# Optimization experiments

Measured on AMD Instinct MI355X. Metric: run time of the kernel, lower is better.

## Reference

```python
import jax, jax.numpy as jnp
import numpy as np

B = 32768   # batch
F = 32      # per-node feature dim
H = 256     # hidden width
M = 4       # modules per node
OUT = 8     # final output dim
INIT_W = 0.003
B_INIT = 0.1


def _lin(k, din, dout):
    # fanin_init-style uniform weights, bias filled with 0.1 (hidden layers)
    s = 1.0 / np.sqrt(din)
    W = jax.random.uniform(k, (M, din, dout), jnp.float32, -s, s)
    b = jnp.full((M, dout), B_INIT, jnp.float32)
    return W, b


def setup_inputs() -> dict:
    key = jax.random.key(0)
    ks = jax.random.split(key, 16)
    feats = jax.random.normal(ks[0], (B, 4 * F), jnp.float32)
    idx = jax.random.randint(ks[1], (B, 4), 0, M)
    onehots = jax.nn.one_hot(idx, M, dtype=jnp.float32).reshape(B, 4 * M)
    input_val = jnp.concatenate([feats, onehots], axis=1)  # [B,144]

    W00, b00 = _lin(ks[2], F, H)        # node0 post layer 0
    W01, b01 = _lin(ks[3], H, H)        # node0 post layer 1
    Wpre1, bpre1 = _lin(ks[4], F, H)    # node1 pre
    Wpost1, bpost1 = _lin(ks[5], 2 * H, H)  # node1 interface (prev 256 + own 256)
    Wpre2, bpre2 = _lin(ks[6], F, H)
    Wpost2, bpost2 = _lin(ks[7], 2 * H, H)
    Wpre3, bpre3 = _lin(ks[8], F, H)
    Wpost3, bpost3 = _lin(ks[9], 2 * H, H)
    # final output layer: uniform(-init_w, init_w) for W and b, identity act
    Wfin3 = jax.random.uniform(ks[10], (M, H, OUT), jnp.float32, -INIT_W, INIT_W)
    bfin3 = jax.random.uniform(ks[11], (M, OUT), jnp.float32, -INIT_W, INIT_W)
    return dict(input_val=input_val,
                W00=W00, b00=b00, W01=W01, b01=b01,
                Wpre1=Wpre1, bpre1=bpre1, Wpost1=Wpost1, bpost1=bpost1,
                Wpre2=Wpre2, bpre2=bpre2, Wpost2=Wpost2, bpost2=bpost2,
                Wpre3=Wpre3, bpre3=bpre3, Wpost3=Wpost3, bpost3=bpost3,
                Wfin3=Wfin3, bfin3=bfin3)


def _select(h, onehot):
    # per-row pick of the assigned module's output: [B,M,D],[B,M] -> [B,D]
    return jnp.einsum('bmo,bm->bo', h, onehot)


def reference(input_val, W00, b00, W01, b01,
              Wpre1, bpre1, Wpost1, bpost1,
              Wpre2, bpre2, Wpost2, bpost2,
              Wpre3, bpre3, Wpost3, bpost3,
              Wfin3, bfin3):
    feat = lambda j: input_val[:, j * F:(j + 1) * F]
    oh = lambda j: input_val[:, 4 * F + j * M: 4 * F + (j + 1) * M]

    # node 0: two hidden layers, module-dispatched (dense-all-modules + one-hot combine)
    h = jax.nn.relu(jnp.einsum('bi,mio->bmo', feat(0), W00) + b00)
    h = jax.nn.relu(jnp.einsum('bmi,mio->bmo', h, W01) + b01)
    x = _select(h, oh(0))  # [B,H]

    def node(x_prev, fj, ohj, Wpre, bpre, Wpost, bpost):
        hp = jax.nn.relu(jnp.einsum('bi,mio->bmo', fj, Wpre) + bpre)
        # interface layer consumes concat([x_prev, hp]); split the weight to
        # avoid materializing [B,M,2H]
        hq = jax.nn.relu(jnp.einsum('bi,mio->bmo', x_prev, Wpost[:, :H, :])
                         + jnp.einsum('bmi,mio->bmo', hp, Wpost[:, H:, :])
                         + bpost)
        return hq  # [B,M,H]

    x = _select(node(x, feat(1), oh(1), Wpre1, bpre1, Wpost1, bpost1), oh(1))
    x = _select(node(x, feat(2), oh(2), Wpre2, bpre2, Wpost2, bpost2), oh(2))

    h3 = node(x, feat(3), oh(3), Wpre3, bpre3, Wpost3, bpost3)  # [B,M,H]
    out = jnp.einsum('bmi,mio->bmo', h3, Wfin3) + bfin3          # final linear, identity act
    return _select(out, oh(3))  # [B,OUT]
```

## Files before the change

kernel.cpp:

```cpp
#include <hip/hip_runtime.h>

#define NB 32768
#define MAXTILE 768
#define ROWS 64
#define NT 4
#define XHS 536

typedef short s8v __attribute__((ext_vector_type(8)));
typedef short s4v __attribute__((ext_vector_type(4)));
typedef float f4v __attribute__((ext_vector_type(4)));
typedef unsigned short u16;
typedef unsigned short u16x4 __attribute__((ext_vector_type(4)));
typedef unsigned int u32;
typedef unsigned char u8;

__device__ __forceinline__ float bf2f(u16 u) { return __uint_as_float(((u32)u) << 16); }
__device__ __forceinline__ u16 f2bf(float f) {
    u32 x = __float_as_uint(f);
    x += 0x7FFFu + ((x >> 16) & 1u);
    return (u16)(x >> 16);
}
__device__ __forceinline__ s8v ld8(const u16* p) { return *reinterpret_cast<const s8v*>(p); }

#define MFMA16(a, b, c) __builtin_amdgcn_mfma_f32_16x16x32_bf16((a), (b), (c), 0, 0, 0)

template <int N> struct IC { static constexpr int v = N; };

__device__ __forceinline__ void detect_flag(const void* input, int tid, int* shflag)
{
    if (tid < 64) {
        u32 w = ((const u32*)input)[tid];
        u32 h0 = w & 0xFFFFu;
        u32 e0 = (h0 >> 7) & 0xFFu;
        bool plaus = (h0 == 0u) || (e0 >= 96u && e0 <= 143u);
        unsigned long long m = __ballot(plaus);
        if (tid == 0) *shflag = (__popcll(m) >= 48) ? 1 : 0;
    }
}

struct RepArgs {
    const void* W01; const void* Wp[3]; const void* pre[4]; const void* fin;
    const void* bias[9];
    u16 *rPre, *rW01, *rWp[3], *rFin, *cbias;
};

__global__ __launch_bounds__(256) void prepA_kernel(const void* __restrict__ inputv,
                                                    int* __restrict__ gcnt,
                                                    int* __restrict__ perm2,
                                                    RepArgs R)
{
    __shared__ int lcnt[256];
    __shared__ int sBase[256];
    __shared__ u16 T[8192];
    __shared__ int shmisc;
    int tid = threadIdx.x;
    int b = blockIdx.x;
    detect_flag(inputv, tid, &shmisc);
    __syncthreads();
    int flag = shmisc;

    if (b < 128) {
        lcnt[tid] = 0;
        __syncthreads();
        int row = (b << 8) + tid;
        const u32* in32 = (const u32*)inputv;
        const u16* in16 = (const u16*)inputv;
        int key = 0;
        if (flag) {
#pragma unroll
            for (int j = 0; j < 4; j++) {
                u16x4 v = *(const u16x4*)(in16 + row * 144 + 128 + j * 4);
                int m = v[1] ? 1 : (v[2] ? 2 : (v[3] ? 3 : 0));
                key |= m << (j << 1);
            }
        } else {
#pragma unroll
            for (int j = 0; j < 4; j++) {
                const u32* p = in32 + row * 144 + 128 + j * 4;
                u32 v1 = p[1], v2 = p[2], v3 = p[3];
                int m = v1 ? 1 : (v2 ? 2 : (v3 ? 3 : 0));
                key |= m << (j << 1);
            }
        }
        int loc = atomicAdd(&lcnt[key], 1);
        __syncthreads();
        int c = lcnt[tid];
        sBase[tid] = c ? atomicAdd(&gcnt[tid], c) : 0;
        __syncthreads();
        int slot = sBase[key] + loc;
        if (slot < 512) perm2[(key << 9) + slot] = row;
        return;
    }

    int rb = b - 128;
    const void* src = nullptr; u16* dst = nullptr; int K = 0, k0 = 0, mrow = 0;
    if (rb < 32) {
        int m = rb >> 3, s = rb & 7;
        src = R.W01; dst = R.rW01 + (m * 8 + s) * 8192; K = 256; k0 = s * 32; mrow = m;
    } else if (rb < 224) {
        int idx = rb - 32, mat = idx >> 6, r = idx & 63, m = r >> 4, s = r & 15;
        src = R.Wp[mat]; dst = R.rWp[mat] + (m * 16 + s) * 8192; K = 512; k0 = s * 32; mrow = m;
    } else if (rb < 240) {
        int idx = rb - 224, mat = idx >> 2, m = idx & 3;
        src = R.pre[mat]; dst = R.rPre + (mat * 4 + m) * 8192; K = 32; k0 = 0; mrow = m;
    } else if (rb < 244) {
        int m = rb - 240;
        const u16* s16 = (const u16*)R.fin;
        const float* s32 = (const float*)R.fin;
        for (int i = tid; i < 2048; i += 256) {
            int si = (m * 256 + (i >> 3)) * 8 + (i & 7);
            T[i] = flag ? s16[si] : f2bf(s32[si]);
        }
        __syncthreads();
        u16* d = R.rFin + m * 4096;
        for (int i = tid; i < 4096; i += 256) {
            int s = i >> 9, lane = (i >> 3) & 63, j = i & 7;
            int q = lane >> 4, l16 = lane & 15;
            int k = s * 32 + q * 8 + j;
            d[i] = (l16 < 8) ? T[k * 8 + l16] : (u16)0;
        }
        return;
    } else {
        const int sz[9] = {1024,1024,1024,1024,1024,1024,1024,1024,32};
        const int of[9] = {0,1024,2048,3072,4096,5120,6144,7168,8192};
        for (int i = tid; i < 8224; i += 256) {
            int t = i, e = 0;
            while (t >= sz[e]) { t -= sz[e]; e++; }
            R.cbias[of[e] + t] = flag ? ((const u16*)R.bias[e])[t]
                                      : f2bf(((const float*)R.bias[e])[t]);
        }
        return;
    }
    const u16* s16 = (const u16*)src;
    const float* s32 = (const float*)src;
    for (int i = tid; i < 8192; i += 256) {
        int k = i >> 8, n = i & 255;
        int srcIdx = (mrow * K + k0 + k) * 256 + n;
        T[i] = flag ? s16[srcIdx] : f2bf(s32[srcIdx]);
    }
    __syncthreads();
    for (int i = tid; i < 8192; i += 256) {
        int mt = i >> 9, lane = (i >> 3) & 63, j = i & 7;
        int k = ((lane >> 4) << 3) + j, n = (mt << 4) + (lane & 15);
        dst[i] = T[(k << 8) + n];
    }
}

struct MainP { const u16 *rPre, *rW01, *rWp1, *rWp2, *rWp3, *rFin, *cbias; };

__global__ __launch_bounds__(512, 4) void main_kernel(
    const void* __restrict__ inRaw,
    const int* __restrict__ gcnt, const int* __restrict__ perm2,
    MainP P, void* __restrict__ outp)
{
    __shared__ __align__(16) u16 xh[ROWS * XHS];
    __shared__ int rowids[ROWS];
    __shared__ int shflag;
    __shared__ int sMeta[4];

    int tid = threadIdx.x;
    int lane = tid & 63, w = tid >> 6, quad = lane >> 4, l16 = lane & 15;

    int b = blockIdx.x;
    int t = ((b & 7) * (MAXTILE / 8)) + (b >> 3);

    detect_flag(inRaw, tid, &shflag);

    if (tid < 64) {
        int4 g = *(const int4*)(gcnt + tid * 4);
        int tot4[4] = {g.x, g.y, g.z, g.w};
        int tiles4[4], lsum = 0;
#pragma unroll
        for (int j = 0; j < 4; j++) { tiles4[j] = (tot4[j] + 63) >> 6; lsum += tiles4[j]; }
        int pre = lsum;
#pragma unroll
        for (int off = 1; off < 64; off <<= 1) {
            int v = __shfl_up(pre, off, 64);
            if (tid >= off) pre += v;
        }
        int run = pre - lsum;
#pragma unroll
        for (int j = 0; j < 4; j++) {
            if (t >= run && t < run + tiles4[j]) {
                sMeta[0] = tid * 4 + j;
                sMeta[1] = t - run;
                sMeta[2] = tot4[j];
            }
            run += tiles4[j];
        }
        if (tid == 63) sMeta[3] = pre;
    }
    __syncthreads();
    if (t >= sMeta[3]) return;
    int key = sMeta[0], tau = sMeta[1], tot = sMeta[2];
    int cntIn = tot - tau * ROWS; if (cntIn > ROWS) cntIn = ROWS;
    if (tid < ROWS) {
        int g = tid < cntIn ? tid : cntIn - 1;
        rowids[tid] = perm2[(key << 9) + tau * ROWS + g];
    }
    __syncthreads();

    int flag = shflag;
    int rows_[NT];
#pragma unroll
    for (int nt = 0; nt < NT; nt++) rows_[nt] = rowids[nt * 16 + l16];

    const u16* in16 = (const u16*)inRaw;
    const float* in32 = (const float*)inRaw;
    int mt0 = w << 1, mt1 = mt0 + 1;

    f4v acc0[NT], acc1[NT];

    auto gemm_run = [&](auto nc, const u16* Ab, int ks0) {
        constexpr int N = decltype(nc)::v;
        constexpr int D = (N > 8) ? 6 : 4;
        const u16* base0 = Ab + mt0 * 512 + lane * 8;
        const u16* base1 = Ab + mt1 * 512 + lane * 8;
        s8v A0[D], A1[D];
#pragma unroll
        for (int d = 0; d < D && d < N; d++) {
            A0[d] = ld8(base0 + d * 8192);
            A1[d] = ld8(base1 + d * 8192);
        }
        __syncthreads();
        __builtin_amdgcn_s_setprio(1);
#pragma unroll
        for (int s = 0; s < N; s++) {
            s8v c0 = A0[s % D], c1 = A1[s % D];
            if (s + D < N) {
                A0[s % D] = ld8(base0 + (s + D) * 8192);
                A1[s % D] = ld8(base1 + (s + D) * 8192);
            }
#pragma unroll
            for (int nt = 0; nt < NT; nt++) {
                s8v B = ld8(&xh[(nt * 16 + l16) * XHS + (ks0 + s) * 32 + quad * 8]);
                acc0[nt] = MFMA16(c0, B, acc0[nt]);
                acc1[nt] = MFMA16(c1, B, acc1[nt]);
            }
        }
        __builtin_amdgcn_s_setprio(0);
    };

    for (int node = 0; node < 4; node++) {
        int m = (key >> (node << 1)) & 3;

        s8v fb[NT];
#pragma unroll
        for (int nt = 0; nt < NT; nt++) {
            int off = rows_[nt] * 144 + (node << 5) + (quad << 3);
            if (flag) fb[nt] = ld8(in16 + off);
            else {
                f4v f0 = *(const f4v*)(in32 + off);
                f4v f1 = *(const f4v*)(in32 + off + 4);
                s8v r;
#pragma unroll
                for (int j = 0; j < 4; j++) { r[j] = (short)f2bf(f0[j]); r[4 + j] = (short)f2bf(f1[j]); }
                fb[nt] = r;
            }
        }

        const u16* preB = P.rPre + ((node << 2) + m) * 8192;
#pragma unroll
        for (int ci = 0; ci < 2; ci++) {
            int mt = mt0 + ci;
            s8v a = ld8(preB + mt * 512 + lane * 8);
            u16x4 bv = *(const u16x4*)(P.cbias + node * 2048 + m * 256 + mt * 16 + quad * 4);
            f4v bias;
#pragma unroll
            for (int r = 0; r < 4; r++) bias[r] = bf2f(bv[r]);
#pragma unroll
            for (int nt = 0; nt < NT; nt++) {
                f4v c = MFMA16(a, fb[nt], bias);
                s4v p;
#pragma unroll
                for (int r = 0; r < 4; r++) { float v = c[r] > 0.f ? c[r] : 0.f; p[r] = (short)f2bf(v); }
                *(s4v*)&xh[(nt * 16 + l16) * XHS + 256 + mt * 16 + quad * 4] = p;
            }
        }

        {
            u16x4 b0 = *(const u16x4*)(P.cbias + node * 2048 + 1024 + m * 256 + mt0 * 16 + quad * 4);
            u16x4 b1 = *(const u16x4*)(P.cbias + node * 2048 + 1024 + m * 256 + mt1 * 16 + quad * 4);
            f4v f0, f1;
#pragma unroll
            for (int r = 0; r < 4; r++) { f0[r] = bf2f(b0[r]); f1[r] = bf2f(b1[r]); }
#pragma unroll
            for (int nt = 0; nt < NT; nt++) { acc0[nt] = f0; acc1[nt] = f1; }
        }

        if (node == 0) gemm_run(IC<8>{},  P.rW01 + m * 8 * 8192, 8);
        else {
            const u16* WB = (node == 1 ? P.rWp1 : (node == 2 ? P.rWp2 : P.rWp3)) + m * 16 * 8192;
            gemm_run(IC<16>{}, WB, 0);
        }
        __syncthreads();

#pragma unroll
        for (int ci = 0; ci < 2; ci++) {
            int mt = mt0 + ci;
#pragma unroll
            for (int nt = 0; nt < NT; nt++) {
                f4v a = ci ? acc1[nt] : acc0[nt];
                s4v p;
#pragma unroll
                for (int r = 0; r < 4; r++) { float v = a[r] > 0.f ? a[r] : 0.f; p[r] = (short)f2bf(v); }
                *(s4v*)&xh[(nt * 16 + l16) * XHS + mt * 16 + quad * 4] = p;
            }
        }
    }
    __syncthreads();

    if (w < NT) {
        int m3 = (key >> 6) & 3;
        f4v c;
#pragma unroll
        for (int r = 0; r < 4; r++)
            c[r] = (quad < 2) ? bf2f(P.cbias[8192 + m3 * 8 + quad * 4 + r]) : 0.f;
#pragma unroll
        for (int s = 0; s < 8; s++) {
            s8v A = ld8(P.rFin + m3 * 4096 + s * 512 + lane * 8);
            s8v B = ld8(&xh[(w * 16 + l16) * XHS + s * 32 + quad * 8]);
            c = MFMA16(A, B, c);
        }
        int bidx = w * 16 + l16;
        if (quad < 2 && bidx < cntIn) {
            int row = rowids[bidx];
            if (flag) {
                s4v p;
#pragma unroll
                for (int r = 0; r < 4; r++) p[r] = (short)f2bf(c[r]);
                *(s4v*)((u16*)outp + row * 8 + quad * 4) = p;
            } else {
                *(f4v*)((float*)outp + row * 8 + quad * 4) = c;
            }
        }
    }
}

extern "C" void kernel_launch(void* const* d_in, const int* in_sizes, int n_in,
                              void* d_out, int out_size, void* d_ws, size_t ws_size,
                              hipStream_t stream)
{
    (void)in_sizes; (void)n_in; (void)out_size;
    const void* input  = d_in[0];
    const void* W00    = d_in[1];
    const void* b00    = d_in[2];
    const void* W01    = d_in[3];
    const void* b01    = d_in[4];
    const void* Wpre1  = d_in[5];
    const void* bpre1  = d_in[6];
    const void* Wpost1 = d_in[7];
    const void* bpost1 = d_in[8];
    const void* Wpre2  = d_in[9];
    const void* bpre2  = d_in[10];
    const void* Wpost2 = d_in[11];
    const void* bpost2 = d_in[12];
    const void* Wpre3  = d_in[13];
    const void* bpre3  = d_in[14];
    const void* Wpost3 = d_in[15];
    const void* bpost3 = d_in[16];
    const void* Wfin   = d_in[17];
    const void* bfin   = d_in[18];

    char* base = (char*)d_ws;
    size_t off = 0;
    auto alloc = [&](size_t bytes) -> char* {
        char* p = base + off;
        off += (bytes + 255) & ~(size_t)255;
        return p;
    };
    int*  gcnt      = (int*)alloc(256 * 4);
    int*  perm2     = (int*)alloc(256 * 512 * 4);
    u16*  cbias    = (u16*)alloc(8224 * 2);
    u16*  rPre     = (u16*)alloc(131072 * 2);
    u16*  rW01     = (u16*)alloc(262144 * 2);
    u16*  rWp1     = (u16*)alloc(524288 * 2);
    u16*  rWp2     = (u16*)alloc(524288 * 2);
    u16*  rWp3     = (u16*)alloc(524288 * 2);
    u16*  rFin     = (u16*)alloc(16384 * 2);
    if (off > ws_size) return;

    RepArgs R;
    R.W01 = W01; R.Wp[0] = Wpost1; R.Wp[1] = Wpost2; R.Wp[2] = Wpost3;
    R.pre[0] = W00; R.pre[1] = Wpre1; R.pre[2] = Wpre2; R.pre[3] = Wpre3;
    R.fin = Wfin;
    R.bias[0] = b00;   R.bias[1] = b01;
    R.bias[2] = bpre1; R.bias[3] = bpost1;
    R.bias[4] = bpre2; R.bias[5] = bpost2;
    R.bias[6] = bpre3; R.bias[7] = bpost3;
    R.bias[8] = bfin;
    R.rPre = rPre; R.rW01 = rW01;
    R.rWp[0] = rWp1; R.rWp[1] = rWp2; R.rWp[2] = rWp3;
    R.rFin = rFin; R.cbias = cbias;

    hipMemsetAsync(gcnt, 0, 256 * 4, stream);
    prepA_kernel<<<373, 256, 0, stream>>>(input, gcnt, perm2, R);

    MainP P;
    P.rPre = rPre; P.rW01 = rW01; P.rWp1 = rWp1; P.rWp2 = rWp2; P.rWp3 = rWp3;
    P.rFin = rFin; P.cbias = cbias;
    main_kernel<<<MAXTILE, 512, 0, stream>>>(input, gcnt, perm2, P, d_out);
}
```

Baseline: 191.3 us.

## Pre-pack bf16 features and store activations in MFMA-fragment LDS layout

```diff
diff --git a/kernel.cpp b/kernel.cpp
--- a/kernel.cpp
+++ b/kernel.cpp
@@ -4,7 +4,6 @@
 #define MAXTILE 768
 #define ROWS 64
 #define NT 4
-#define XHS 536
 
 typedef short s8v __attribute__((ext_vector_type(8)));
 typedef short s4v __attribute__((ext_vector_type(4)));
@@ -47,6 +46,7 @@
 __global__ __launch_bounds__(256) void prepA_kernel(const void* __restrict__ inputv,
                                                     int* __restrict__ gcnt,
                                                     int* __restrict__ perm2,
+                                                    u16* __restrict__ feats16,
                                                     RepArgs R)
 {
     __shared__ int lcnt[256];
@@ -89,6 +89,23 @@
         __syncthreads();
         int slot = sBase[key] + loc;
         if (slot < 512) perm2[(key << 9) + slot] = row;
+
+        int r0 = b << 8;
+        if (flag) {
+            for (int i = tid; i < 256 * 16; i += 256) {
+                int r = r0 + (i >> 4), j = (i & 15) << 3;
+                *(s8v*)(feats16 + ((size_t)r << 7) + j) = ld8(in16 + (size_t)r * 144 + j);
+            }
+        } else {
+            for (int i = tid; i < 256 * 32; i += 256) {
+                int r = r0 + (i >> 5), j = (i & 31) << 2;
+                f4v f = *(const f4v*)(in32 + (size_t)r * 144 + j);
+                s4v p;
+#pragma unroll
+                for (int q = 0; q < 4; q++) p[q] = (short)f2bf(f[q]);
+                *(s4v*)(feats16 + ((size_t)r << 7) + j) = p;
+            }
+        }
         return;
     }
 
@@ -146,14 +163,14 @@
     }
 }
 
-struct MainP { const u16 *rPre, *rW01, *rWp1, *rWp2, *rWp3, *rFin, *cbias; };
+struct MainP { const u16 *rPre, *rW01, *rWp1, *rWp2, *rWp3, *rFin, *cbias, *feats; };
 
 __global__ __launch_bounds__(512, 4) void main_kernel(
     const void* __restrict__ inRaw,
     const int* __restrict__ gcnt, const int* __restrict__ perm2,
     MainP P, void* __restrict__ outp)
 {
-    __shared__ __align__(16) u16 xh[ROWS * XHS];
+    __shared__ __align__(16) u16 xhB[32768];
     __shared__ int rowids[ROWS];
     __shared__ int shflag;
     __shared__ int sMeta[4];
@@ -205,15 +222,15 @@
 #pragma unroll
     for (int nt = 0; nt < NT; nt++) rows_[nt] = rowids[nt * 16 + l16];
 
-    const u16* in16 = (const u16*)inRaw;
-    const float* in32 = (const float*)inRaw;
+    const u16* feats = P.feats;
     int mt0 = w << 1, mt1 = mt0 + 1;
+    int stA = ((quad >> 1) * 16 + l16) * 8 + (quad & 1) * 4;
 
     f4v acc0[NT], acc1[NT];
 
     auto gemm_run = [&](auto nc, const u16* Ab, int ks0) {
         constexpr int N = decltype(nc)::v;
-        constexpr int D = (N > 8) ? 6 : 4;
+        constexpr int D = 4;
         const u16* base0 = Ab + mt0 * 512 + lane * 8;
         const u16* base1 = Ab + mt1 * 512 + lane * 8;
         s8v A0[D], A1[D];
@@ -233,7 +250,7 @@
             }
 #pragma unroll
             for (int nt = 0; nt < NT; nt++) {
-                s8v B = ld8(&xh[(nt * 16 + l16) * XHS + (ks0 + s) * 32 + quad * 8]);
+                s8v B = ld8(&xhB[((nt * 16 + ks0 + s) << 9) + lane * 8]);
                 acc0[nt] = MFMA16(c0, B, acc0[nt]);
                 acc1[nt] = MFMA16(c1, B, acc1[nt]);
             }
@@ -246,18 +263,8 @@
 
         s8v fb[NT];
 #pragma unroll
-        for (int nt = 0; nt < NT; nt++) {
-            int off = rows_[nt] * 144 + (node << 5) + (quad << 3);
-            if (flag) fb[nt] = ld8(in16 + off);
-            else {
-                f4v f0 = *(const f4v*)(in32 + off);
-                f4v f1 = *(const f4v*)(in32 + off + 4);
-                s8v r;
-#pragma unroll
-                for (int j = 0; j < 4; j++) { r[j] = (short)f2bf(f0[j]); r[4 + j] = (short)f2bf(f1[j]); }
-                fb[nt] = r;
-            }
-        }
+        for (int nt = 0; nt < NT; nt++)
+            fb[nt] = ld8(feats + ((size_t)rows_[nt] << 7) + (node << 5) + (quad << 3));
 
         const u16* preB = P.rPre + ((node << 2) + m) * 8192;
 #pragma unroll
@@ -274,7 +281,7 @@
                 s4v p;
 #pragma unroll
                 for (int r = 0; r < 4; r++) { float v = c[r] > 0.f ? c[r] : 0.f; p[r] = (short)f2bf(v); }
-                *(s4v*)&xh[(nt * 16 + l16) * XHS + 256 + mt * 16 + quad * 4] = p;
+                *(s4v*)&xhB[(((nt * 16 + 8 + w) << 9)) + ci * 256 + stA] = p;
             }
         }
 
@@ -297,14 +304,13 @@
 
 #pragma unroll
         for (int ci = 0; ci < 2; ci++) {
-            int mt = mt0 + ci;
 #pragma unroll
             for (int nt = 0; nt < NT; nt++) {
                 f4v a = ci ? acc1[nt] : acc0[nt];
                 s4v p;
 #pragma unroll
                 for (int r = 0; r < 4; r++) { float v = a[r] > 0.f ? a[r] : 0.f; p[r] = (short)f2bf(v); }
-                *(s4v*)&xh[(nt * 16 + l16) * XHS + mt * 16 + quad * 4] = p;
+                *(s4v*)&xhB[((nt * 16 + w) << 9) + ci * 256 + stA] = p;
             }
         }
     }
@@ -319,7 +325,7 @@
 #pragma unroll
         for (int s = 0; s < 8; s++) {
             s8v A = ld8(P.rFin + m3 * 4096 + s * 512 + lane * 8);
-            s8v B = ld8(&xh[(w * 16 + l16) * XHS + s * 32 + quad * 8]);
+            s8v B = ld8(&xhB[((w * 16 + s) << 9) + lane * 8]);
             c = MFMA16(A, B, c);
         }
         int bidx = w * 16 + l16;
@@ -371,6 +377,7 @@
     };
     int*  gcnt      = (int*)alloc(256 * 4);
     int*  perm2     = (int*)alloc(256 * 512 * 4);
+    u16*  feats16   = (u16*)alloc((size_t)NB * 128 * 2);
     u16*  cbias    = (u16*)alloc(8224 * 2);
     u16*  rPre     = (u16*)alloc(131072 * 2);
     u16*  rW01     = (u16*)alloc(262144 * 2);
@@ -394,10 +401,10 @@
     R.rFin = rFin; R.cbias = cbias;
 
     hipMemsetAsync(gcnt, 0, 256 * 4, stream);
-    prepA_kernel<<<373, 256, 0, stream>>>(input, gcnt, perm2, R);
+    prepA_kernel<<<373, 256, 0, stream>>>(input, gcnt, perm2, feats16, R);
 
     MainP P;
     P.rPre = rPre; P.rW01 = rW01; P.rWp1 = rWp1; P.rWp2 = rWp2; P.rWp3 = rWp3;
-    P.rFin = rFin; P.cbias = cbias;
+    P.rFin = rFin; P.cbias = cbias; P.feats = feats16;
     main_kernel<<<MAXTILE, 512, 0, stream>>>(input, gcnt, perm2, P, d_out);
 }
```

New measurement: 190.1 us (median of 2 runs). No clear change (-0.6%).
